# Performance work log

Measured on AMD Instinct MI355X. Metric: run time of the kernel, lower is better.

The kernel has to match this reference:

```python
import jax, jax.numpy as jnp
import numpy as np

N_NODES = 100000


def _gcn_layer(x, W, b, src, dst, n):
    # symmetric normalization (add_self_loops=False): deg = in-degree at dst
    deg = jax.ops.segment_sum(jnp.ones_like(src, dtype=x.dtype), dst, num_segments=n)
    dis = jnp.where(deg > 0, jax.lax.rsqrt(jnp.maximum(deg, 1.0)), 0.0)
    h = x @ W                                    # [N, out]
    norm = dis[src] * dis[dst]                   # [E]
    msg = h[src] * norm[:, None]                 # [E, out]
    out = jax.ops.segment_sum(msg, dst, num_segments=n)
    return out + b


def setup_inputs() -> dict:
    key = jax.random.key(0)
    k1, k2, k3, k4, k5, k6 = jax.random.split(key, 6)
    F_IN, HID, OUT = 64, 64, 2
    x = jax.random.normal(k1, (N_NODES, F_IN), dtype=jnp.float32)
    edge_index = jax.random.randint(k2, (2, 1600000), 0, N_NODES, dtype=jnp.int64)
    s1 = 1.0 / np.sqrt(2 * F_IN)
    s2 = 1.0 / np.sqrt(HID)
    W1 = jax.random.uniform(k3, (2 * F_IN, HID), jnp.float32, -s1, s1)
    b1 = jax.random.uniform(k4, (HID,), jnp.float32, -s1, s1)
    W2 = jax.random.uniform(k5, (HID, OUT), jnp.float32, -s2, s2)
    b2 = jax.random.uniform(k6, (OUT,), jnp.float32, -s2, s2)
    return {"x": x, "edge_index": edge_index, "W1": W1, "b1": b1, "W2": W2, "b2": b2}


def reference(x, edge_index, W1, b1, W2, b2):
    n = x.shape[0]
    src, dst = edge_index[0], edge_index[1]
    # global mean pool broadcast to every node, concat on feature dim -> [N, 2F]
    mean = jnp.mean(x, axis=0, keepdims=True)
    complete = jnp.concatenate([x, jnp.broadcast_to(mean, x.shape)], axis=1)
    h = _gcn_layer(complete, W1, b1, src, dst, n)
    h = jax.nn.relu(h)
    out = _gcn_layer(h, W2, b2, src, dst, n)
    return out
```

## Files before the change

### kernel.cpp

```cpp
#include <hip/hip_runtime.h>


#define NPB        256
#define NPB_SHIFT  8
#define BKTS       512
#define BKT_CAP    5120
#define CHUNK      8192
#define EPT        16
#define CS_BLK     128
#define CUR_STRIDE 32

using bf16x8 = __attribute__((ext_vector_type(8))) short;
using f32x4  = __attribute__((ext_vector_type(4))) float;

__device__ __forceinline__ unsigned short f2bf(float v) {
    unsigned u = __float_as_uint(v);
    u += 0x7FFFu + ((u >> 16) & 1u);
    return (unsigned short)(u >> 16);
}
__device__ __forceinline__ float bfu_lo(unsigned u) { return __uint_as_float(u << 16); }
__device__ __forceinline__ float bfu_hi(unsigned u) { return __uint_as_float(u & 0xFFFF0000u); }

__global__ __launch_bounds__(512) void bucketAC_kernel(
        const int* __restrict__ src, const int* __restrict__ dst,
        int e, unsigned* __restrict__ pairs, int* __restrict__ cursor,
        const float* __restrict__ x, float* __restrict__ sums,
        const float* __restrict__ W1, unsigned short* __restrict__ wtg,
        unsigned short* __restrict__ xbf, int n) {
    int tid = threadIdx.x;
    if (blockIdx.x < CS_BLK) {
        __shared__ float4 s4[512];
        int cb = blockIdx.x;
        const float4* x4 = (const float4*)x;
        int total4 = n * 16;
        float4 acc = make_float4(0.f, 0.f, 0.f, 0.f);
        for (int i = cb * 512 + tid; i < total4; i += CS_BLK * 512) {
            float4 v = x4[i];
            acc.x += v.x; acc.y += v.y; acc.z += v.z; acc.w += v.w;
            ushort4 hv;
            hv.x = f2bf(v.x); hv.y = f2bf(v.y); hv.z = f2bf(v.z); hv.w = f2bf(v.w);
            *(ushort4*)&xbf[(size_t)i * 4] = hv;
        }
        s4[tid] = acc;
        __syncthreads();
        if (tid < 16) {
            float4 v = s4[tid];
            for (int k = 1; k < 32; ++k) {
                float4 w = s4[tid + 16 * k];
                v.x += w.x; v.y += w.y; v.z += w.z; v.w += w.w;
            }
            atomicAdd(&sums[tid * 4 + 0], v.x);
            atomicAdd(&sums[tid * 4 + 1], v.y);
            atomicAdd(&sums[tid * 4 + 2], v.z);
            atomicAdd(&sums[tid * 4 + 3], v.w);
        }
        return;
    }
    if (blockIdx.x == CS_BLK) {
        for (int i = tid; i < 4096; i += 512) {
            int k = i >> 6, j = i & 63;
            wtg[j * 64 + k] = f2bf(W1[k * 64 + j]);
        }
        return;
    }
    __shared__ int cnt[BKTS], gpos[BKTS];
    __shared__ int wsumA[8];
    __shared__ unsigned stage[CHUNK];
    __shared__ unsigned short bb[CHUNK];
    int chunkStart = (blockIdx.x - CS_BLK - 1) * CHUNK;
    int v = e - chunkStart;
    if (v > CHUNK) v = CHUNK;
    cnt[tid] = 0;
    __syncthreads();
    int myb[EPT], myoff[EPT];
    unsigned myp[EPT];
#pragma unroll
    for (int t = 0; t < EPT; ++t) {
        int i = chunkStart + t * 512 + tid;
        myb[t] = -1;
        if (i < e) {
            int s = src[i], d = dst[i];
            myb[t] = d >> NPB_SHIFT;
            myp[t] = ((unsigned)s << NPB_SHIFT) | (unsigned)(d & (NPB - 1));
            myoff[t] = atomicAdd(&cnt[myb[t]], 1);
        }
    }
    __syncthreads();
    int lane = tid & 63, wvi = tid >> 6;
    int myCnt = cnt[tid];
    int sv = myCnt;
#pragma unroll
    for (int off = 1; off < 64; off <<= 1) {
        int t = __shfl_up(sv, off, 64);
        if (lane >= off) sv += t;
    }
    if (lane == 63) wsumA[wvi] = sv;
    __syncthreads();
    int wbase = 0;
#pragma unroll
    for (int k = 0; k < 8; ++k) if (k < wvi) wbase += wsumA[k];
    int excl = sv + wbase - myCnt;
    if (myCnt > 0) {
        int gb = atomicAdd(&cursor[tid * CUR_STRIDE], myCnt);
        gpos[tid] = tid * BKT_CAP + gb - excl;
    }
    cnt[tid] = excl;
    __syncthreads();
#pragma unroll
    for (int t = 0; t < EPT; ++t) {
        if (myb[t] >= 0) {
            int p = cnt[myb[t]] + myoff[t];
            stage[p] = myp[t];
            bb[p] = (unsigned short)myb[t];
        }
    }
    __syncthreads();
    for (int j = tid; j < v; j += 512) {
        int bk = bb[j];
        int wi = gpos[bk] + j;
        if (wi < (bk + 1) * BKT_CAP) pairs[wi] = stage[j];
    }
}

__global__ __launch_bounds__(512) void csrBG_kernel(
        const unsigned* __restrict__ pairs, const int* __restrict__ cursor,
        float* __restrict__ dis, int* __restrict__ rowstart,
        int* __restrict__ eidx, int n,
        const float* __restrict__ sums, const float* __restrict__ W1,
        const unsigned short* __restrict__ wtg, const unsigned short* __restrict__ xbf,
        unsigned short* __restrict__ h1s) {
    __shared__ int ldeg[NPB];
    __shared__ int lcur[NPB];
    __shared__ int wred[8], wsum[8];
    __shared__ __align__(16) float cv[64];
    __shared__ __align__(16) char smem[BKT_CAP * 8];
    unsigned* pl = (unsigned*)smem;
    int* el = (int*)(smem + BKT_CAP * 4);
    unsigned short* Ws = (unsigned short*)smem;
    unsigned short* Xs = (unsigned short*)(smem + 64 * 72 * 2);
    float* disl = (float*)ldeg;
    int b = blockIdx.x;
    int tid = threadIdx.x;
    int lane = tid & 63;
    int wvi = tid >> 6;
    int node0 = b << NPB_SHIFT;
    int nl = n - node0;
    if (nl > NPB) nl = NPB;
    int cnt_b = cursor[b * CUR_STRIDE];
    if (cnt_b > BKT_CAP) cnt_b = BKT_CAP;
    if (tid < NPB) ldeg[tid] = 0;
    int c = (tid < b) ? cursor[tid * CUR_STRIDE] : 0;
#pragma unroll
    for (int off = 1; off < 64; off <<= 1) c += __shfl_xor(c, off, 64);
    if (lane == 0) wred[wvi] = c;
    __syncthreads();
    const unsigned* mp = pairs + (size_t)b * BKT_CAP;
    for (int i = tid; i < cnt_b; i += 512) {
        unsigned p = mp[i];
        pl[i] = p;
        atomicAdd(&ldeg[p & (NPB - 1)], 1);
    }
    int ebase = 0;
#pragma unroll
    for (int k = 0; k < 8; ++k) ebase += wred[k];
    __syncthreads();
    int mydeg = (tid < NPB) ? ldeg[tid] : 0;
    int sv = mydeg;
#pragma unroll
    for (int off = 1; off < 64; off <<= 1) {
        int t = __shfl_up(sv, off, 64);
        if (lane >= off) sv += t;
    }
    if (lane == 63) wsum[wvi] = sv;
    __syncthreads();
    int wbase = 0;
#pragma unroll
    for (int k = 0; k < 8; ++k) if (k < wvi) wbase += wsum[k];
    int excl = sv + wbase - mydeg;
    if (tid < NPB) {
        lcur[tid] = excl;
        if (tid < nl) rowstart[node0 + tid] = ebase + excl;
        float dv = mydeg > 0 ? rsqrtf((float)mydeg) : 0.f;
        disl[tid] = dv;
        if (tid < nl) dis[node0 + tid] = dv;
    }
    if (tid == 0 && node0 + NPB >= n)
        rowstart[n] = ebase + cnt_b;
    __syncthreads();
    for (int i = tid; i < cnt_b; i += 512) {
        unsigned p = pl[i];
        int pos = atomicAdd(&lcur[p & (NPB - 1)], 1);
        el[pos] = (int)(p >> NPB_SHIFT);
    }
    __syncthreads();
    for (int i = tid; i < cnt_b; i += 512)
        eidx[ebase + i] = el[i];
    if (tid < 64) {
        float inv_n = 1.0f / (float)n;
        float acc = 0.f;
        for (int k = 0; k < 64; ++k) acc += (sums[k] * inv_n) * W1[(64 + k) * 64 + tid];
        cv[tid] = acc;
    }
    __syncthreads();
    for (int i = tid; i < 1024; i += 512) {
        int j = i >> 4, k4 = (i & 15) * 4;
        *(ushort4*)&Ws[j * 72 + k4] = *(const ushort4*)&wtg[j * 64 + k4];
    }
    int wv = wvi;
    int tile = wv >> 2;
    int w4 = wv & 3;
    int l15 = lane & 15;
    int quad = lane >> 4;
#pragma unroll
    for (int it = 0; it < 2; ++it) {
        __syncthreads();
        for (int i = tid; i < 1024; i += 512) {
            int r = i >> 3, c8 = (i & 7) * 8;
            int gr = node0 + it * 128 + r;
            bf16x8 hv = {0, 0, 0, 0, 0, 0, 0, 0};
            if (gr < n) hv = *(const bf16x8*)&xbf[(size_t)gr * 64 + c8];
            *(bf16x8*)&Xs[((r >> 6) ? 64 * 72 : 0) + (r & 63) * 72 + c8] = hv;
        }
        __syncthreads();
        int xrow = w4 * 16 + l15;
        f32x4 acc0 = {0.f, 0.f, 0.f, 0.f}, acc1 = acc0, acc2 = acc0, acc3 = acc0;
#pragma unroll
        for (int ks = 0; ks < 2; ++ks) {
            bf16x8 bfrag = *(const bf16x8*)&Xs[(tile ? 64 * 72 : 0) + xrow * 72 + ks * 32 + quad * 8];
            bf16x8 a0 = *(const bf16x8*)&Ws[(0 * 16 + l15) * 72 + ks * 32 + quad * 8];
            bf16x8 a1 = *(const bf16x8*)&Ws[(1 * 16 + l15) * 72 + ks * 32 + quad * 8];
            bf16x8 a2 = *(const bf16x8*)&Ws[(2 * 16 + l15) * 72 + ks * 32 + quad * 8];
            bf16x8 a3 = *(const bf16x8*)&Ws[(3 * 16 + l15) * 72 + ks * 32 + quad * 8];
            acc0 = __builtin_amdgcn_mfma_f32_16x16x32_bf16(a0, bfrag, acc0, 0, 0, 0);
            acc1 = __builtin_amdgcn_mfma_f32_16x16x32_bf16(a1, bfrag, acc1, 0, 0, 0);
            acc2 = __builtin_amdgcn_mfma_f32_16x16x32_bf16(a2, bfrag, acc2, 0, 0, 0);
            acc3 = __builtin_amdgcn_mfma_f32_16x16x32_bf16(a3, bfrag, acc3, 0, 0, 0);
        }
        int lrow = it * 128 + tile * 64 + xrow;
        int grow = node0 + lrow;
        if (grow < n) {
            float dv = disl[lrow];
            const float4* c4 = (const float4*)cv;
            f32x4 accs[4] = {acc0, acc1, acc2, acc3};
#pragma unroll
            for (int t = 0; t < 4; ++t) {
                float4 cj = c4[t * 4 + quad];
                ushort4 hs;
                hs.x = f2bf((accs[t][0] + cj.x) * dv);
                hs.y = f2bf((accs[t][1] + cj.y) * dv);
                hs.z = f2bf((accs[t][2] + cj.z) * dv);
                hs.w = f2bf((accs[t][3] + cj.w) * dv);
                *(ushort4*)&h1s[(size_t)grow * 64 + t * 16 + quad * 4] = hs;
            }
        }
    }
}

__global__ void gather1_kernel(const int* __restrict__ rowstart,
                               const int* __restrict__ eidx, const float* __restrict__ dis,
                               const unsigned short* __restrict__ h1s,
                               const float* __restrict__ b1, const float* __restrict__ W2,
                               float* __restrict__ h2s, int n) {
    int lane = threadIdx.x & 63;
    int node = blockIdx.x * 4 + (threadIdx.x >> 6);
    if (node >= n) return;
    int rs = rowstart[node];
    int re = rowstart[node + 1];
    int dn = re - rs;
    int m = dn < 64 ? dn : 64;
    int eHeld = (lane < m) ? eidx[rs + lane] : 0;
    int sub = lane >> 5;
    int fp  = (lane & 31) * 2;
    float ax = 0.f, ay = 0.f;
    int j = 0;
    for (; j + 16 <= m; j += 16) {
        int s0 = __shfl(eHeld, j + 0 + sub, 64);
        int s1 = __shfl(eHeld, j + 2 + sub, 64);
        int s2 = __shfl(eHeld, j + 4 + sub, 64);
        int s3 = __shfl(eHeld, j + 6 + sub, 64);
        int s4 = __shfl(eHeld, j + 8 + sub, 64);
        int s5 = __shfl(eHeld, j + 10 + sub, 64);
        int s6 = __shfl(eHeld, j + 12 + sub, 64);
        int s7 = __shfl(eHeld, j + 14 + sub, 64);
        unsigned u0 = *(const unsigned*)&h1s[((size_t)s0 << 6) + fp];
        unsigned u1 = *(const unsigned*)&h1s[((size_t)s1 << 6) + fp];
        unsigned u2 = *(const unsigned*)&h1s[((size_t)s2 << 6) + fp];
        unsigned u3 = *(const unsigned*)&h1s[((size_t)s3 << 6) + fp];
        unsigned u4 = *(const unsigned*)&h1s[((size_t)s4 << 6) + fp];
        unsigned u5 = *(const unsigned*)&h1s[((size_t)s5 << 6) + fp];
        unsigned u6 = *(const unsigned*)&h1s[((size_t)s6 << 6) + fp];
        unsigned u7 = *(const unsigned*)&h1s[((size_t)s7 << 6) + fp];
        ax += (bfu_lo(u0) + bfu_lo(u1)) + (bfu_lo(u2) + bfu_lo(u3))
            + (bfu_lo(u4) + bfu_lo(u5)) + (bfu_lo(u6) + bfu_lo(u7));
        ay += (bfu_hi(u0) + bfu_hi(u1)) + (bfu_hi(u2) + bfu_hi(u3))
            + (bfu_hi(u4) + bfu_hi(u5)) + (bfu_hi(u6) + bfu_hi(u7));
    }
    for (; j + 8 <= m; j += 8) {
        int s0 = __shfl(eHeld, j + 0 + sub, 64);
        int s1 = __shfl(eHeld, j + 2 + sub, 64);
        int s2 = __shfl(eHeld, j + 4 + sub, 64);
        int s3 = __shfl(eHeld, j + 6 + sub, 64);
        unsigned u0 = *(const unsigned*)&h1s[((size_t)s0 << 6) + fp];
        unsigned u1 = *(const unsigned*)&h1s[((size_t)s1 << 6) + fp];
        unsigned u2 = *(const unsigned*)&h1s[((size_t)s2 << 6) + fp];
        unsigned u3 = *(const unsigned*)&h1s[((size_t)s3 << 6) + fp];
        ax += (bfu_lo(u0) + bfu_lo(u1)) + (bfu_lo(u2) + bfu_lo(u3));
        ay += (bfu_hi(u0) + bfu_hi(u1)) + (bfu_hi(u2) + bfu_hi(u3));
    }
    for (; j + 4 <= m; j += 4) {
        int s0 = __shfl(eHeld, j + 0 + sub, 64);
        int s1 = __shfl(eHeld, j + 2 + sub, 64);
        unsigned u0 = *(const unsigned*)&h1s[((size_t)s0 << 6) + fp];
        unsigned u1 = *(const unsigned*)&h1s[((size_t)s1 << 6) + fp];
        ax += bfu_lo(u0) + bfu_lo(u1);
        ay += bfu_hi(u0) + bfu_hi(u1);
    }
    for (; j < m; j += 2) {
        int jj = j + sub;
        int s = __shfl(eHeld, jj < m ? jj : 0, 64);
        if (jj < m) {
            unsigned u = *(const unsigned*)&h1s[((size_t)s << 6) + fp];
            ax += bfu_lo(u);
            ay += bfu_hi(u);
        }
    }
    for (int t = 64; t < dn; ++t) {
        if (sub == 0) {
            int s = eidx[rs + t];
            unsigned u = *(const unsigned*)&h1s[((size_t)s << 6) + fp];
            ax += bfu_lo(u);
            ay += bfu_hi(u);
        }
    }
    ax += __shfl_xor(ax, 32, 64);
    ay += __shfl_xor(ay, 32, 64);
    float di = dis[node];
    float2 bv = ((const float2*)b1)[lane & 31];
    float4 w = ((const float4*)W2)[lane & 31];
    float t0 = fmaxf(di * ax + bv.x, 0.f);
    float t1 = fmaxf(di * ay + bv.y, 0.f);
    float v0 = t0 * w.x + t1 * w.z;
    float v1 = t0 * w.y + t1 * w.w;
#pragma unroll
    for (int off = 1; off <= 16; off <<= 1) {
        v0 += __shfl_xor(v0, off, 64);
        v1 += __shfl_xor(v1, off, 64);
    }
    if (lane == 0) {
        h2s[(size_t)node * 2 + 0] = di * v0;
        h2s[(size_t)node * 2 + 1] = di * v1;
    }
}

__global__ void gather2_kernel(const int* __restrict__ rowstart,
                               const int* __restrict__ eidx, const float* __restrict__ dis,
                               const float2* __restrict__ h2s, const float* __restrict__ b2,
                               float2* __restrict__ out, int n) {
    int tid = threadIdx.x;
    int node = blockIdx.x * 16 + (tid >> 4);
    if (node >= n) return;
    int el = tid & 15;
    int rs = rowstart[node];
    int dn = rowstart[node + 1] - rs;
    float ax = 0.f, ay = 0.f;
    for (int t = el; t < dn; t += 16) {
        int s = eidx[rs + t];
        float2 h = h2s[s];
        ax += h.x;
        ay += h.y;
    }
#pragma unroll
    for (int off = 1; off <= 8; off <<= 1) {
        ax += __shfl_xor(ax, off, 64);
        ay += __shfl_xor(ay, off, 64);
    }
    if (el == 0) {
        float di = dis[node];
        out[node] = make_float2(di * ax + b2[0], di * ay + b2[1]);
    }
}

extern "C" void kernel_launch(void* const* d_in, const int* in_sizes, int n_in,
                              void* d_out, int out_size, void* d_ws, size_t ws_size,
                              hipStream_t stream) {
    const float* x  = (const float*)d_in[0];
    const int*   ei = (const int*)d_in[1];
    const float* W1 = (const float*)d_in[2];
    const float* b1 = (const float*)d_in[3];
    const float* W2 = (const float*)d_in[4];
    const float* b2 = (const float*)d_in[5];
    float2* out = (float2*)d_out;

    const int n = in_sizes[0] / 64;
    const int e = in_sizes[1] / 2;
    const int* srcI = ei;
    const int* dstI = ei + e;
    const int nbkt = (n + NPB - 1) >> NPB_SHIFT;

    char* p = (char*)d_ws;
    int* rowstart = (int*)p;    p += ((size_t)(n + 1) * 4 + 255) & ~255ull;
    float* dis    = (float*)p;  p += ((size_t)n * 4 + 255) & ~255ull;
    float* sums   = (float*)p;
    int* cursor   = (int*)(p + 256);
    size_t zsize  = 256 + (size_t)nbkt * CUR_STRIDE * 4;
    char* zbase   = p;          p += (zsize + 255) & ~255ull;
    unsigned short* wtg = (unsigned short*)p;  p += (4096 * 2 + 255) & ~255ull;
    unsigned short* xbf = (unsigned short*)p;  p += ((size_t)n * 64 * 2 + 255) & ~255ull;
    int* eidx     = (int*)p;    p += ((size_t)e * 4 + 255) & ~255ull;
    unsigned* pairs = (unsigned*)p;  p += ((size_t)nbkt * BKT_CAP * 4 + 255) & ~255ull;
    unsigned short* h1s = (unsigned short*)p;  p += ((size_t)n * 64 * 2 + 255) & ~255ull;
    float* h2s    = (float*)p;

    hipMemsetAsync(zbase, 0, zsize, stream);

    const int nchunks = (e + CHUNK - 1) / CHUNK;

    bucketAC_kernel<<<CS_BLK + 1 + nchunks, 512, 0, stream>>>(srcI, dstI, e, pairs, cursor,
                                                              x, sums, W1, wtg, xbf, n);
    csrBG_kernel<<<nbkt, 512, 0, stream>>>(pairs, cursor, dis, rowstart, eidx, n,
                                           sums, W1, wtg, xbf, h1s);
    gather1_kernel<<<(n + 3) / 4, 256, 0, stream>>>(rowstart, eidx, dis, h1s, b1, W2, h2s, n);
    gather2_kernel<<<(n + 15) / 16, 256, 0, stream>>>(rowstart, eidx, dis, (const float2*)h2s,
                                                      b2, out, n);
}
```

Before: 173.9 us.

## Compute per-node degrees globally and build rowstart via separate scan kernels

Degree counting moves into the bucketing kernel as global atomics per destination node. Two new small kernels then compute the block sums and the exclusive prefix scan, which produce rowstart and dis. The CSR build kernel reads these instead of recounting degrees and rescanning the cursor array in every block. This takes a serial prefix over the buckets and the local degree atomics off the CSR kernel, at the cost of 1.6M global atomics, two extra launches and a larger memset.

Measured after the change: 231.0 us. +32.9%, slower.

```diff
diff --git a/kernel.cpp b/kernel.cpp
--- a/kernel.cpp
+++ b/kernel.cpp
@@ -24,6 +24,7 @@
 __global__ __launch_bounds__(512) void bucketAC_kernel(
         const int* __restrict__ src, const int* __restrict__ dst,
         int e, unsigned* __restrict__ pairs, int* __restrict__ cursor,
+        int* __restrict__ deg,
         const float* __restrict__ x, float* __restrict__ sums,
         const float* __restrict__ W1, unsigned short* __restrict__ wtg,
         unsigned short* __restrict__ xbf, int n) {
@@ -83,6 +84,7 @@
             myb[t] = d >> NPB_SHIFT;
             myp[t] = ((unsigned)s << NPB_SHIFT) | (unsigned)(d & (NPB - 1));
             myoff[t] = atomicAdd(&cnt[myb[t]], 1);
+            atomicAdd(&deg[d], 1);
         }
     }
     __syncthreads();
@@ -122,75 +124,89 @@
     }
 }
 
+__global__ __launch_bounds__(256) void scan1_kernel(
+        const int* __restrict__ deg, int* __restrict__ bsum, int n) {
+    __shared__ int ws[4];
+    int b = blockIdx.x, tid = threadIdx.x;
+    int gid = (b << NPB_SHIFT) + tid;
+    int v = (gid < n) ? deg[gid] : 0;
+#pragma unroll
+    for (int off = 1; off < 64; off <<= 1) v += __shfl_xor(v, off, 64);
+    if ((tid & 63) == 0) ws[tid >> 6] = v;
+    __syncthreads();
+    if (tid == 0) bsum[b] = ws[0] + ws[1] + ws[2] + ws[3];
+}
+
+__global__ __launch_bounds__(256) void scan2_kernel(
+        const int* __restrict__ deg, const int* __restrict__ bsum,
+        int* __restrict__ rowstart, float* __restrict__ dis, int n) {
+    __shared__ int ws[4], sb[4];
+    int b = blockIdx.x, tid = threadIdx.x;
+    int lane = tid & 63, wvi = tid >> 6;
+    int gid = (b << NPB_SHIFT) + tid;
+    int c = 0;
+    for (int k = tid; k < b; k += 256) c += bsum[k];
+#pragma unroll
+    for (int off = 1; off < 64; off <<= 1) c += __shfl_xor(c, off, 64);
+    if (lane == 0) sb[wvi] = c;
+    int v = (gid < n) ? deg[gid] : 0;
+    int sv = v;
+#pragma unroll
+    for (int off = 1; off < 64; off <<= 1) {
+        int t = __shfl_up(sv, off, 64);
+        if (lane >= off) sv += t;
+    }
+    if (lane == 63) ws[wvi] = sv;
+    __syncthreads();
+    int ebase = sb[0] + sb[1] + sb[2] + sb[3];
+    int wbase = 0;
+#pragma unroll
+    for (int k = 0; k < 4; ++k) if (k < wvi) wbase += ws[k];
+    int excl = ebase + wbase + sv - v;
+    if (gid < n) {
+        rowstart[gid] = excl;
+        dis[gid] = (v > 0) ? rsqrtf((float)v) : 0.f;
+    } else if (gid == n) {
+        rowstart[n] = excl;
+    }
+}
+
 __global__ __launch_bounds__(512) void csrBG_kernel(
-        const unsigned* __restrict__ pairs, const int* __restrict__ cursor,
-        float* __restrict__ dis, int* __restrict__ rowstart,
-        int* __restrict__ eidx, int n,
+        const unsigned* __restrict__ pairs, const int* __restrict__ rowstart,
+        const float* __restrict__ dis, int* __restrict__ eidx, int n,
         const float* __restrict__ sums, const float* __restrict__ W1,
         const unsigned short* __restrict__ wtg, const unsigned short* __restrict__ xbf,
         unsigned short* __restrict__ h1s) {
-    __shared__ int ldeg[NPB];
     __shared__ int lcur[NPB];
-    __shared__ int wred[8], wsum[8];
+    __shared__ float disl[NPB];
     __shared__ __align__(16) float cv[64];
     __shared__ __align__(16) char smem[BKT_CAP * 8];
     unsigned* pl = (unsigned*)smem;
     int* el = (int*)(smem + BKT_CAP * 4);
     unsigned short* Ws = (unsigned short*)smem;
     unsigned short* Xs = (unsigned short*)(smem + 64 * 72 * 2);
-    float* disl = (float*)ldeg;
     int b = blockIdx.x;
     int tid = threadIdx.x;
     int lane = tid & 63;
-    int wvi = tid >> 6;
     int node0 = b << NPB_SHIFT;
     int nl = n - node0;
     if (nl > NPB) nl = NPB;
-    int cnt_b = cursor[b * CUR_STRIDE];
+    int ebase = rowstart[node0];
+    int eend  = rowstart[node0 + NPB <= n ? node0 + NPB : n];
+    int cnt_b = eend - ebase;
     if (cnt_b > BKT_CAP) cnt_b = BKT_CAP;
-    if (tid < NPB) ldeg[tid] = 0;
-    int c = (tid < b) ? cursor[tid * CUR_STRIDE] : 0;
-#pragma unroll
-    for (int off = 1; off < 64; off <<= 1) c += __shfl_xor(c, off, 64);
-    if (lane == 0) wred[wvi] = c;
-    __syncthreads();
+    if (tid < NPB) {
+        int g = node0 + tid;
+        lcur[tid] = (tid < nl) ? (rowstart[g] - ebase) : cnt_b;
+        disl[tid] = (tid < nl) ? dis[g] : 0.f;
+    }
     const unsigned* mp = pairs + (size_t)b * BKT_CAP;
-    for (int i = tid; i < cnt_b; i += 512) {
-        unsigned p = mp[i];
-        pl[i] = p;
-        atomicAdd(&ldeg[p & (NPB - 1)], 1);
-    }
-    int ebase = 0;
-#pragma unroll
-    for (int k = 0; k < 8; ++k) ebase += wred[k];
-    __syncthreads();
-    int mydeg = (tid < NPB) ? ldeg[tid] : 0;
-    int sv = mydeg;
-#pragma unroll
-    for (int off = 1; off < 64; off <<= 1) {
-        int t = __shfl_up(sv, off, 64);
-        if (lane >= off) sv += t;
-    }
-    if (lane == 63) wsum[wvi] = sv;
-    __syncthreads();
-    int wbase = 0;
-#pragma unroll
-    for (int k = 0; k < 8; ++k) if (k < wvi) wbase += wsum[k];
-    int excl = sv + wbase - mydeg;
-    if (tid < NPB) {
-        lcur[tid] = excl;
-        if (tid < nl) rowstart[node0 + tid] = ebase + excl;
-        float dv = mydeg > 0 ? rsqrtf((float)mydeg) : 0.f;
-        disl[tid] = dv;
-        if (tid < nl) dis[node0 + tid] = dv;
-    }
-    if (tid == 0 && node0 + NPB >= n)
-        rowstart[n] = ebase + cnt_b;
+    for (int i = tid; i < cnt_b; i += 512) pl[i] = mp[i];
     __syncthreads();
     for (int i = tid; i < cnt_b; i += 512) {
         unsigned p = pl[i];
         int pos = atomicAdd(&lcur[p & (NPB - 1)], 1);
-        el[pos] = (int)(p >> NPB_SHIFT);
+        if (pos < BKT_CAP) el[pos] = (int)(p >> NPB_SHIFT);
     }
     __syncthreads();
     for (int i = tid; i < cnt_b; i += 512)
@@ -206,7 +222,7 @@
         int j = i >> 4, k4 = (i & 15) * 4;
         *(ushort4*)&Ws[j * 72 + k4] = *(const ushort4*)&wtg[j * 64 + k4];
     }
-    int wv = wvi;
+    int wv = tid >> 6;
     int tile = wv >> 2;
     int w4 = wv & 3;
     int l15 = lane & 15;
@@ -396,14 +412,17 @@
     const int* srcI = ei;
     const int* dstI = ei + e;
     const int nbkt = (n + NPB - 1) >> NPB_SHIFT;
+    const int nbkt2 = (n + NPB) >> NPB_SHIFT;
 
     char* p = (char*)d_ws;
     int* rowstart = (int*)p;    p += ((size_t)(n + 1) * 4 + 255) & ~255ull;
     float* dis    = (float*)p;  p += ((size_t)n * 4 + 255) & ~255ull;
-    float* sums   = (float*)p;
-    int* cursor   = (int*)(p + 256);
-    size_t zsize  = 256 + (size_t)nbkt * CUR_STRIDE * 4;
+    int* deg      = (int*)p;
+    float* sums   = (float*)(p + (size_t)n * 4);
+    int* cursor   = (int*)(p + (size_t)n * 4 + 256);
+    size_t zsize  = (size_t)n * 4 + 256 + (size_t)nbkt * CUR_STRIDE * 4;
     char* zbase   = p;          p += (zsize + 255) & ~255ull;
+    int* bsum     = (int*)p;    p += ((size_t)nbkt * 4 + 255) & ~255ull;
     unsigned short* wtg = (unsigned short*)p;  p += (4096 * 2 + 255) & ~255ull;
     unsigned short* xbf = (unsigned short*)p;  p += ((size_t)n * 64 * 2 + 255) & ~255ull;
     int* eidx     = (int*)p;    p += ((size_t)e * 4 + 255) & ~255ull;
@@ -416,8 +435,10 @@
     const int nchunks = (e + CHUNK - 1) / CHUNK;
 
     bucketAC_kernel<<<CS_BLK + 1 + nchunks, 512, 0, stream>>>(srcI, dstI, e, pairs, cursor,
-                                                              x, sums, W1, wtg, xbf, n);
-    csrBG_kernel<<<nbkt, 512, 0, stream>>>(pairs, cursor, dis, rowstart, eidx, n,
+                                                              deg, x, sums, W1, wtg, xbf, n);
+    scan1_kernel<<<nbkt, 256, 0, stream>>>(deg, bsum, n);
+    scan2_kernel<<<nbkt2, 256, 0, stream>>>(deg, bsum, rowstart, dis, n);
+    csrBG_kernel<<<nbkt, 512, 0, stream>>>(pairs, rowstart, dis, eidx, n,
                                            sums, W1, wtg, xbf, h1s);
     gather1_kernel<<<(n + 3) / 4, 256, 0, stream>>>(rowstart, eidx, dis, h1s, b1, W2, h2s, n);
     gather2_kernel<<<(n + 15) / 16, 256, 0, stream>>>(rowstart, eidx, dis, (const float2*)h2s,
```

## Replace global bucket cursor atomics with per-chunk offset matrix

Applied to the files above, without the earlier changes.

The bucketing kernel no longer claims space per bucket with global atomicAdd on a strided cursor array. Each chunk now writes its locally bucket-sorted edges contiguously and records per-bucket exclusive offsets into an offset matrix. The CSR kernel rebuilds each bucket by prefix-summing run lengths across chunks and gathering the small runs from every chunk. Chunk size is halved, and the cursor memset plus the staging bucket-id array are removed. In exchange, the CSR stage performs many short, scattered reads (one run per chunk per bucket) with low lane utilisation, and the design assumes there are no more than 512 chunks.

Measured after the change: 192.9 us. 1.11x slower.

```diff
diff --git a/kernel.cpp b/kernel.cpp
--- a/kernel.cpp
+++ b/kernel.cpp
@@ -5,10 +5,9 @@
 #define NPB_SHIFT  8
 #define BKTS       512
 #define BKT_CAP    5120
-#define CHUNK      8192
-#define EPT        16
+#define CHUNK      4096
+#define EPT        8
 #define CS_BLK     128
-#define CUR_STRIDE 32
 
 using bf16x8 = __attribute__((ext_vector_type(8))) short;
 using f32x4  = __attribute__((ext_vector_type(4))) float;
@@ -23,7 +22,7 @@
 
 __global__ __launch_bounds__(512) void bucketAC_kernel(
         const int* __restrict__ src, const int* __restrict__ dst,
-        int e, unsigned* __restrict__ pairs, int* __restrict__ cursor,
+        int e, unsigned* __restrict__ pairs, int* __restrict__ offmat,
         const float* __restrict__ x, float* __restrict__ sums,
         const float* __restrict__ W1, unsigned short* __restrict__ wtg,
         unsigned short* __restrict__ xbf, int n) {
@@ -63,11 +62,11 @@
         }
         return;
     }
-    __shared__ int cnt[BKTS], gpos[BKTS];
+    __shared__ int cnt[BKTS];
     __shared__ int wsumA[8];
     __shared__ unsigned stage[CHUNK];
-    __shared__ unsigned short bb[CHUNK];
-    int chunkStart = (blockIdx.x - CS_BLK - 1) * CHUNK;
+    int chunkIdx = blockIdx.x - CS_BLK - 1;
+    int chunkStart = chunkIdx * CHUNK;
     int v = e - chunkStart;
     if (v > CHUNK) v = CHUNK;
     cnt[tid] = 0;
@@ -100,30 +99,21 @@
 #pragma unroll
     for (int k = 0; k < 8; ++k) if (k < wvi) wbase += wsumA[k];
     int excl = sv + wbase - myCnt;
-    if (myCnt > 0) {
-        int gb = atomicAdd(&cursor[tid * CUR_STRIDE], myCnt);
-        gpos[tid] = tid * BKT_CAP + gb - excl;
-    }
+    offmat[chunkIdx * BKTS + tid] = excl;
     cnt[tid] = excl;
     __syncthreads();
 #pragma unroll
     for (int t = 0; t < EPT; ++t) {
-        if (myb[t] >= 0) {
-            int p = cnt[myb[t]] + myoff[t];
-            stage[p] = myp[t];
-            bb[p] = (unsigned short)myb[t];
-        }
-    }
-    __syncthreads();
-    for (int j = tid; j < v; j += 512) {
-        int bk = bb[j];
-        int wi = gpos[bk] + j;
-        if (wi < (bk + 1) * BKT_CAP) pairs[wi] = stage[j];
-    }
+        if (myb[t] >= 0)
+            stage[cnt[myb[t]] + myoff[t]] = myp[t];
+    }
+    __syncthreads();
+    for (int j = tid; j < v; j += 512)
+        pairs[chunkStart + j] = stage[j];
 }
 
 __global__ __launch_bounds__(512) void csrBG_kernel(
-        const unsigned* __restrict__ pairs, const int* __restrict__ cursor,
+        const unsigned* __restrict__ pairs, const int* __restrict__ offmat, int nch,
         float* __restrict__ dis, int* __restrict__ rowstart,
         int* __restrict__ eidx, int n,
         const float* __restrict__ sums, const float* __restrict__ W1,
@@ -135,7 +125,10 @@
     __shared__ __align__(16) float cv[64];
     __shared__ __align__(16) char smem[BKT_CAP * 8];
     unsigned* pl = (unsigned*)smem;
-    int* el = (int*)(smem + BKT_CAP * 4);
+    int* el    = (int*)(smem + BKT_CAP * 4);
+    int* runst = el;
+    int* plb   = el + 512;
+    int* rln   = el + 1024;
     unsigned short* Ws = (unsigned short*)smem;
     unsigned short* Xs = (unsigned short*)(smem + 64 * 72 * 2);
     float* disl = (float*)ldeg;
@@ -146,23 +139,49 @@
     int node0 = b << NPB_SHIFT;
     int nl = n - node0;
     if (nl > NPB) nl = NPB;
-    int cnt_b = cursor[b * CUR_STRIDE];
+    if (tid < NPB) ldeg[tid] = 0;
+    int o0 = 0, len = 0;
+    if (tid < nch) {
+        o0 = offmat[tid * BKTS + b];
+        int o1 = offmat[tid * BKTS + b + 1];
+        len = o1 - o0;
+    }
+    int c2 = o0;
+#pragma unroll
+    for (int off = 1; off < 64; off <<= 1) c2 += __shfl_xor(c2, off, 64);
+    if (lane == 0) wred[wvi] = c2;
+    int svl = len;
+#pragma unroll
+    for (int off = 1; off < 64; off <<= 1) {
+        int t = __shfl_up(svl, off, 64);
+        if (lane >= off) svl += t;
+    }
+    if (lane == 63) wsum[wvi] = svl;
+    __syncthreads();
+    int ebase = 0, cnt_b = 0;
+#pragma unroll
+    for (int k = 0; k < 8; ++k) { ebase += wred[k]; cnt_b += wsum[k]; }
+    int wb2 = 0;
+#pragma unroll
+    for (int k = 0; k < 8; ++k) if (k < wvi) wb2 += wsum[k];
     if (cnt_b > BKT_CAP) cnt_b = BKT_CAP;
-    if (tid < NPB) ldeg[tid] = 0;
-    int c = (tid < b) ? cursor[tid * CUR_STRIDE] : 0;
-#pragma unroll
-    for (int off = 1; off < 64; off <<= 1) c += __shfl_xor(c, off, 64);
-    if (lane == 0) wred[wvi] = c;
-    __syncthreads();
-    const unsigned* mp = pairs + (size_t)b * BKT_CAP;
-    for (int i = tid; i < cnt_b; i += 512) {
-        unsigned p = mp[i];
-        pl[i] = p;
-        atomicAdd(&ldeg[p & (NPB - 1)], 1);
-    }
-    int ebase = 0;
-#pragma unroll
-    for (int k = 0; k < 8; ++k) ebase += wred[k];
+    if (tid < nch) {
+        runst[tid] = tid * CHUNK + o0;
+        plb[tid]   = svl + wb2 - len;
+        rln[tid]   = len;
+    }
+    __syncthreads();
+    for (int c = wvi; c < nch; c += 8) {
+        int st = runst[c], base = plb[c], L = rln[c];
+        for (int k = lane; k < L; k += 64) {
+            int pos = base + k;
+            if (pos < BKT_CAP) {
+                unsigned rec = pairs[st + k];
+                pl[pos] = rec;
+                atomicAdd(&ldeg[rec & (NPB - 1)], 1);
+            }
+        }
+    }
     __syncthreads();
     int mydeg = (tid < NPB) ? ldeg[tid] : 0;
     int sv = mydeg;
@@ -396,28 +415,25 @@
     const int* srcI = ei;
     const int* dstI = ei + e;
     const int nbkt = (n + NPB - 1) >> NPB_SHIFT;
+    const int nch  = (e + CHUNK - 1) / CHUNK;
 
     char* p = (char*)d_ws;
     int* rowstart = (int*)p;    p += ((size_t)(n + 1) * 4 + 255) & ~255ull;
     float* dis    = (float*)p;  p += ((size_t)n * 4 + 255) & ~255ull;
-    float* sums   = (float*)p;
-    int* cursor   = (int*)(p + 256);
-    size_t zsize  = 256 + (size_t)nbkt * CUR_STRIDE * 4;
-    char* zbase   = p;          p += (zsize + 255) & ~255ull;
+    float* sums   = (float*)p;  p += 256;
+    int* offmat   = (int*)p;    p += ((size_t)nch * BKTS * 4 + 255) & ~255ull;
     unsigned short* wtg = (unsigned short*)p;  p += (4096 * 2 + 255) & ~255ull;
     unsigned short* xbf = (unsigned short*)p;  p += ((size_t)n * 64 * 2 + 255) & ~255ull;
     int* eidx     = (int*)p;    p += ((size_t)e * 4 + 255) & ~255ull;
-    unsigned* pairs = (unsigned*)p;  p += ((size_t)nbkt * BKT_CAP * 4 + 255) & ~255ull;
+    unsigned* pairs = (unsigned*)p;  p += ((size_t)e * 4 + 255) & ~255ull;
     unsigned short* h1s = (unsigned short*)p;  p += ((size_t)n * 64 * 2 + 255) & ~255ull;
     float* h2s    = (float*)p;
 
-    hipMemsetAsync(zbase, 0, zsize, stream);
-
-    const int nchunks = (e + CHUNK - 1) / CHUNK;
-
-    bucketAC_kernel<<<CS_BLK + 1 + nchunks, 512, 0, stream>>>(srcI, dstI, e, pairs, cursor,
-                                                              x, sums, W1, wtg, xbf, n);
-    csrBG_kernel<<<nbkt, 512, 0, stream>>>(pairs, cursor, dis, rowstart, eidx, n,
+    hipMemsetAsync(sums, 0, 256, stream);
+
+    bucketAC_kernel<<<CS_BLK + 1 + nch, 512, 0, stream>>>(srcI, dstI, e, pairs, offmat,
+                                                          x, sums, W1, wtg, xbf, n);
+    csrBG_kernel<<<nbkt, 512, 0, stream>>>(pairs, offmat, nch, dis, rowstart, eidx, n,
                                            sums, W1, wtg, xbf, h1s);
     gather1_kernel<<<(n + 3) / 4, 256, 0, stream>>>(rowstart, eidx, dis, h1s, b1, W2, h2s, n);
     gather2_kernel<<<(n + 15) / 16, 256, 0, stream>>>(rowstart, eidx, dis, (const float2*)h2s,
```
